# Kernel optimization log

Hardware: AMD Instinct MI355X
Metric: run time of the kernel (lower is better)

The kernel has to match this reference:

```python
import jax, jax.numpy as jnp
import numpy as np

N_S = 4096      # number of sentences
N_K = 8192      # number of knowledge entries
HID = 1024      # settings.hidden_dim
SENT = 1024     # settings.sent_dim


def setup_inputs() -> dict:
    key = jax.random.key(0)
    ks = jax.random.split(key, 6)
    sentences = jax.random.normal(ks[0], (N_S, SENT), dtype=jnp.float32)
    knowledge = jax.random.normal(ks[1], (N_K, 3 * HID), dtype=jnp.float32)
    # Linear params stored as [in, out] for x @ W + b
    Ws = jax.random.normal(ks[2], (SENT, HID), dtype=jnp.float32) * 0.02
    bs = jnp.zeros((HID,), dtype=jnp.float32)
    Wk = jax.random.normal(ks[3], (3 * HID, HID), dtype=jnp.float32) * 0.02
    bk = jnp.zeros((HID,), dtype=jnp.float32)
    return {"sentences": sentences, "knowledge": knowledge,
            "Ws": Ws, "bs": bs, "Wk": Wk, "bk": bk}


def reference(sentences, knowledge, Ws, bs, Wk, bk):
    S = sentences @ Ws + bs                  # [N_s, h]
    K = knowledge @ Wk + bk                  # [N_k, h]
    align_scores = S @ K.T                   # [N_s, N_k]
    # NOTE: softmax over dim=0 (sentence axis), exactly as the torch module
    attentions = jax.nn.softmax(align_scores, axis=0)
    fused = attentions @ knowledge           # [N_s, 3h]
    return (fused, attentions)
```

## Files before the change

kernel.cpp:

```cpp
#include <hip/hip_runtime.h>
#include <hip/hip_bf16.h>
#include <cstdint>
#include <cstddef>

#define N_S 4096
#define N_Kn 8192
#define HID 1024
#define SENT 1024
#define K3 3072

typedef __attribute__((ext_vector_type(4))) float f4;
typedef __attribute__((ext_vector_type(8))) short bf8;
typedef __attribute__((ext_vector_type(4))) short bf4;
typedef unsigned short u16;

__device__ __forceinline__ u16 f2bf(float x) {
    __hip_bfloat16 h = __float2bfloat16(x);
    return __builtin_bit_cast(u16, h);
}
__device__ __forceinline__ float bf2f(u16 u) {
    union { unsigned int u; float f; } v; v.u = ((unsigned int)u) << 16;
    return v.f;
}

__device__ __forceinline__ void gl16(const u16* g, u16* l) {
    __builtin_amdgcn_global_load_lds(
        (const __attribute__((address_space(1))) void*)g,
        (__attribute__((address_space(3))) void*)l, 16, 0, 0);
}

__device__ __forceinline__ int xcd_swz(int bid, int nwg) {
    const int cpx = nwg >> 3;
    return (bid & 7) * cpx + (bid >> 3);
}


__global__ __launch_bounds__(256) void transpose_split_f32(
    const float* __restrict__ in, u16* __restrict__ hi, u16* __restrict__ lo,
    int R, int C)
{
    __shared__ float tile[32][33];
    const int bx = blockIdx.x * 32, by = blockIdx.y * 32;
    const int tx = threadIdx.x & 31, ty = threadIdx.x >> 5;
#pragma unroll
    for (int i = 0; i < 32; i += 8)
        tile[ty + i][tx] = in[(size_t)(by + ty + i) * C + bx + tx];
    __syncthreads();
#pragma unroll
    for (int i = 0; i < 32; i += 8) {
        const float v = tile[tx][ty + i];
        const u16 h = f2bf(v);
        const size_t o = (size_t)(bx + ty + i) * R + by + tx;
        hi[o] = h;
        lo[o] = f2bf(v - bf2f(h));
    }
}

__global__ __launch_bounds__(256) void transpose_f32_bf16(
    const float* __restrict__ in, u16* __restrict__ out, int R, int C)
{
    __shared__ float tile[32][33];
    const int bx = blockIdx.x * 32, by = blockIdx.y * 32;
    const int tx = threadIdx.x & 31, ty = threadIdx.x >> 5;
#pragma unroll
    for (int i = 0; i < 32; i += 8)
        tile[ty + i][tx] = in[(size_t)(by + ty + i) * C + bx + tx];
    __syncthreads();
#pragma unroll
    for (int i = 0; i < 32; i += 8)
        out[(size_t)(bx + ty + i) * R + by + tx] = f2bf(tile[tx][ty + i]);
}

__global__ __launch_bounds__(256) void gemm_pipe(
    const u16* __restrict__ A, const u16* __restrict__ B,
    float* __restrict__ C, int N, int Kd, int gx)
{
    __shared__ u16 sA[2][4096];
    __shared__ u16 sB[2][4096];

    const int swz = xcd_swz(blockIdx.x, gridDim.x);
    const int bx = swz % gx, by = swz / gx;

    const int t = threadIdx.x;
    const int w = t >> 6, l = t & 63;
    const long brow = (long)by * 128, bcol = (long)bx * 128;
    const int grow = l >> 2;
    const int gcol = ((l & 3) ^ ((l >> 3) & 3)) * 8;

    const int wr = (w >> 1) * 64, wc = (w & 1) * 64;
    const int fr = l & 15, kg = l >> 4;
    const int kq = (kg ^ ((fr >> 1) & 3)) * 8;

    const u16* gA0 = A + (brow + w * 16 + grow) * (long)Kd + gcol;
    const u16* gA1 = A + (brow + 64 + w * 16 + grow) * (long)Kd + gcol;
    const u16* gB0 = B + (bcol + w * 16 + grow) * (long)Kd + gcol;
    const u16* gB1 = B + (bcol + 64 + w * 16 + grow) * (long)Kd + gcol;
    const int lb0 = w * 512, lb1 = 2048 + w * 512;

    f4 acc[4][4];
#pragma unroll
    for (int m = 0; m < 4; m++)
#pragma unroll
        for (int n = 0; n < 4; n++) acc[m][n] = (f4){0.f, 0.f, 0.f, 0.f};

    const int nkt = Kd >> 5;

    gl16(gA0, &sA[0][lb0]); gl16(gA1, &sA[0][lb1]);
    gl16(gB0, &sB[0][lb0]); gl16(gB1, &sB[0][lb1]);
    asm volatile("s_waitcnt vmcnt(0)" ::: "memory");
    __builtin_amdgcn_s_barrier();
    asm volatile("" ::: "memory");

    int cur = 0;
    for (int kt = 0; kt < nkt; ++kt) {
        if (kt + 1 < nkt) {
            const long ko = (long)(kt + 1) * 32;
            const int nx = cur ^ 1;
            gl16(gA0 + ko, &sA[nx][lb0]); gl16(gA1 + ko, &sA[nx][lb1]);
            gl16(gB0 + ko, &sB[nx][lb0]); gl16(gB1 + ko, &sB[nx][lb1]);
        }

        bf8 fa[4], fb[4];
#pragma unroll
        for (int m = 0; m < 4; ++m) {
            fa[m] = *(bf8*)&sA[cur][(wr + m * 16 + fr) * 32 + kq];
            fb[m] = *(bf8*)&sB[cur][(wc + m * 16 + fr) * 32 + kq];
        }
#pragma unroll
        for (int m = 0; m < 4; ++m)
#pragma unroll
            for (int n = 0; n < 4; ++n)
                acc[m][n] = __builtin_amdgcn_mfma_f32_16x16x32_bf16(fa[m], fb[n], acc[m][n], 0, 0, 0);

        asm volatile("s_waitcnt vmcnt(0)" ::: "memory");
        __builtin_amdgcn_s_barrier();
        asm volatile("" ::: "memory");
        cur ^= 1;
    }

#pragma unroll
    for (int n = 0; n < 4; ++n) {
        const long c = bcol + wc + n * 16 + fr;
#pragma unroll
        for (int m = 0; m < 4; ++m) {
            const long r0 = brow + wr + m * 16 + kg * 4;
#pragma unroll
            for (int r = 0; r < 4; ++r)
                C[(r0 + r) * (long)N + c] = acc[m][n][r];
        }
    }
}

template <bool SPLIT, bool AF32, bool EPIS>
__global__ __launch_bounds__(256) void gemm_mfma(
    const void* __restrict__ Aany, const u16* __restrict__ Alo_,
    const u16* __restrict__ Bhi_, const u16* __restrict__ Blo_,
    float* __restrict__ Cf, u16* __restrict__ Chi, u16* __restrict__ Clo,
    const float* __restrict__ bias, int N, int Kd, int gx)
{
    constexpr int SA = AF32 ? 48 : 32;
    __shared__ u16 sAh[128 * SA];
    __shared__ u16 sAl[SPLIT ? 128 * SA : 8];
    __shared__ u16 sBh[128 * 32];
    __shared__ u16 sBl[SPLIT ? 128 * 32 : 8];

    const int swz = xcd_swz(blockIdx.x, gridDim.x);
    const int bxi = swz % gx, byi = swz / gx;

    const int t = threadIdx.x;
    const int w = t >> 6;
    const int l = t & 63;
    const long brow = (long)byi * 128;
    const long bcol = (long)bxi * 128;

    const int grow = l >> 2;
    const int gcol = ((l & 3) ^ ((l >> 3) & 3)) * 8;

    const int wr = (w >> 1) * 64;
    const int wc = (w & 1) * 64;
    const int fr = l & 15;
    const int kg = l >> 4;
    const int kq = (kg ^ ((fr >> 1) & 3)) * 8;

    f4 acc[4][4];
#pragma unroll
    for (int m = 0; m < 4; m++)
#pragma unroll
        for (int n = 0; n < 4; n++) acc[m][n] = (f4){0.f, 0.f, 0.f, 0.f};

    const int nkt = Kd >> 5;
    for (int kt = 0; kt < nkt; ++kt) {
        const int k0 = kt * 32;

#pragma unroll
        for (int i = 0; i < 2; ++i) {
            const long r = bcol + i * 64 + w * 16 + grow;
            const int lb = i * 2048 + w * 512;
            gl16(Bhi_ + r * Kd + k0 + gcol, sBh + lb);
            if constexpr (SPLIT) gl16(Blo_ + r * Kd + k0 + gcol, sBl + lb);
        }

        if constexpr (!AF32) {
            const u16* Ahi = (const u16*)Aany;
#pragma unroll
            for (int i = 0; i < 2; ++i) {
                const long r = brow + i * 64 + w * 16 + grow;
                const int lb = i * 2048 + w * 512;
                gl16(Ahi + r * Kd + k0 + gcol, sAh + lb);
                if constexpr (SPLIT) gl16(Alo_ + r * Kd + k0 + gcol, sAl + lb);
            }
        } else {
            const float* Af = (const float*)Aany;
            const int ar = w * 8 + (l >> 3);
            const int cF = (l & 7) * 4;
#pragma unroll
            for (int j = 0; j < 4; ++j) {
                const int r = j * 32 + ar;
                const f4 v = *(const f4*)(Af + (brow + r) * (long)Kd + k0 + cF);
                u16 h[4], lw[4];
#pragma unroll
                for (int q = 0; q < 4; ++q) {
                    h[q] = f2bf(v[q]);
                    if constexpr (SPLIT) lw[q] = f2bf(v[q] - bf2f(h[q]));
                }
                *(bf4*)&sAh[r * SA + cF] = *(bf4*)h;
                if constexpr (SPLIT) *(bf4*)&sAl[r * SA + cF] = *(bf4*)lw;
            }
        }
        __syncthreads();

        bf8 fah[4], fbh[4], fal[4], fbl[4];
#pragma unroll
        for (int m = 0; m < 4; ++m) {
            if constexpr (AF32) {
                fah[m] = *(bf8*)&sAh[(wr + m * 16 + fr) * SA + kg * 8];
                if constexpr (SPLIT) fal[m] = *(bf8*)&sAl[(wr + m * 16 + fr) * SA + kg * 8];
            } else {
                fah[m] = *(bf8*)&sAh[(wr + m * 16 + fr) * 32 + kq];
                if constexpr (SPLIT) fal[m] = *(bf8*)&sAl[(wr + m * 16 + fr) * 32 + kq];
            }
            fbh[m] = *(bf8*)&sBh[(wc + m * 16 + fr) * 32 + kq];
            if constexpr (SPLIT) fbl[m] = *(bf8*)&sBl[(wc + m * 16 + fr) * 32 + kq];
        }
#pragma unroll
        for (int m = 0; m < 4; ++m)
#pragma unroll
            for (int n = 0; n < 4; ++n) {
                acc[m][n] = __builtin_amdgcn_mfma_f32_16x16x32_bf16(fah[m], fbh[n], acc[m][n], 0, 0, 0);
                if constexpr (SPLIT) {
                    acc[m][n] = __builtin_amdgcn_mfma_f32_16x16x32_bf16(fah[m], fbl[n], acc[m][n], 0, 0, 0);
                    acc[m][n] = __builtin_amdgcn_mfma_f32_16x16x32_bf16(fal[m], fbh[n], acc[m][n], 0, 0, 0);
                }
            }
        __syncthreads();
    }

#pragma unroll
    for (int n = 0; n < 4; ++n) {
        const long c = bcol + wc + n * 16 + fr;
        float bv = 0.f;
        if constexpr (EPIS) bv = bias[c];
#pragma unroll
        for (int m = 0; m < 4; ++m) {
            const long r0 = brow + wr + m * 16 + kg * 4;
#pragma unroll
            for (int r = 0; r < 4; ++r) {
                const float v = acc[m][n][r] + bv;
                if constexpr (EPIS) {
                    const u16 h = f2bf(v);
                    Chi[(r0 + r) * (long)N + c] = h;
                    Clo[(r0 + r) * (long)N + c] = f2bf(v - bf2f(h));
                } else {
                    Cf[(r0 + r) * (long)N + c] = v;
                }
            }
        }
    }
}

#define RCHUNK 128

__global__ __launch_bounds__(256) void softmax_partial(
    const float* __restrict__ align, float* __restrict__ pm, float* __restrict__ ps)
{
    const int col = blockIdx.x * 256 + threadIdx.x;
    const int r0 = blockIdx.y * RCHUNK;
    float m = -3.4e38f;
    for (int r = 0; r < RCHUNK; r++)
        m = fmaxf(m, align[(size_t)(r0 + r) * N_Kn + col]);
    float s = 0.f;
    for (int r = 0; r < RCHUNK; r++)
        s += __expf(align[(size_t)(r0 + r) * N_Kn + col] - m);
    pm[(size_t)blockIdx.y * N_Kn + col] = m;
    ps[(size_t)blockIdx.y * N_Kn + col] = s;
}

__global__ __launch_bounds__(256) void softmax_combine(
    const float* __restrict__ pm, const float* __restrict__ ps,
    float* __restrict__ fm, float* __restrict__ fsinv)
{
    const int col = blockIdx.x * 256 + threadIdx.x;
    float m = -3.4e38f;
#pragma unroll
    for (int i = 0; i < 32; i++) m = fmaxf(m, pm[(size_t)i * N_Kn + col]);
    float s = 0.f;
#pragma unroll
    for (int i = 0; i < 32; i++)
        s += ps[(size_t)i * N_Kn + col] * __expf(pm[(size_t)i * N_Kn + col] - m);
    fm[col] = m;
    fsinv[col] = 1.f / s;
}

__global__ __launch_bounds__(256) void softmax_norm(
    float* __restrict__ align, u16* __restrict__ abf,
    const float* __restrict__ fm, const float* __restrict__ fsinv)
{
    const int col = blockIdx.x * 256 + threadIdx.x;
    const int r0 = blockIdx.y * RCHUNK;
    const float m = fm[col], si = fsinv[col];
    for (int r = 0; r < RCHUNK; r++) {
        const size_t idx = (size_t)(r0 + r) * N_Kn + col;
        const float v = __expf(align[idx] - m) * si;
        align[idx] = v;
        abf[idx] = f2bf(v);
    }
}

extern "C" void kernel_launch(void* const* d_in, const int* in_sizes, int n_in,
                              void* d_out, int out_size, void* d_ws, size_t ws_size,
                              hipStream_t stream)
{
    const float* sentences = (const float*)d_in[0];
    const float* knowledge = (const float*)d_in[1];
    const float* Ws = (const float*)d_in[2];
    const float* bs = (const float*)d_in[3];
    const float* Wk = (const float*)d_in[4];
    const float* bk = (const float*)d_in[5];

    float* out_fused = (float*)d_out;
    float* out_attn = (float*)d_out + (size_t)N_S * K3;

    char* w = (char*)d_ws;
    u16* attn_bf = (u16*)w;
    u16* WsT_hi = (u16*)w; w += (size_t)HID * SENT * 2;
    u16* WsT_lo = (u16*)w; w += (size_t)HID * SENT * 2;
    u16* WkT_hi = (u16*)w; w += (size_t)HID * K3 * 2;
    u16* WkT_lo = (u16*)w; w += (size_t)HID * K3 * 2;
    u16* S_hi   = (u16*)w; w += (size_t)N_S * HID * 2;
    u16* S_lo   = (u16*)w; w += (size_t)N_S * HID * 2;
    u16* K_hi   = (u16*)w; w += (size_t)N_Kn * HID * 2;
    u16* K_lo   = (u16*)w; w += (size_t)N_Kn * HID * 2;
    u16* kT     = (u16*)w; w += (size_t)K3 * N_Kn * 2;
    float* pm   = (float*)w; w += (size_t)32 * N_Kn * 4;
    float* ps   = (float*)w; w += (size_t)32 * N_Kn * 4;
    float* fm   = (float*)w; w += (size_t)N_Kn * 4;
    float* fsv  = (float*)w; w += (size_t)N_Kn * 4;

    transpose_split_f32<<<dim3(HID / 32, SENT / 32), 256, 0, stream>>>(Ws, WsT_hi, WsT_lo, SENT, HID);
    transpose_split_f32<<<dim3(HID / 32, K3 / 32), 256, 0, stream>>>(Wk, WkT_hi, WkT_lo, K3, HID);
    transpose_f32_bf16<<<dim3(K3 / 32, N_Kn / 32), 256, 0, stream>>>(knowledge, kT, N_Kn, K3);

    gemm_mfma<true, true, true><<<(HID / 128) * (N_S / 128), 256, 0, stream>>>(
        sentences, nullptr, WsT_hi, WsT_lo, nullptr, S_hi, S_lo, bs, HID, SENT, HID / 128);

    gemm_mfma<true, true, true><<<(HID / 128) * (N_Kn / 128), 256, 0, stream>>>(
        knowledge, nullptr, WkT_hi, WkT_lo, nullptr, K_hi, K_lo, bk, HID, K3, HID / 128);

    gemm_mfma<true, false, false><<<(N_Kn / 128) * (N_S / 128), 256, 0, stream>>>(
        S_hi, S_lo, K_hi, K_lo, out_attn, nullptr, nullptr, nullptr, N_Kn, HID, N_Kn / 128);

    softmax_partial<<<dim3(N_Kn / 256, N_S / RCHUNK), 256, 0, stream>>>(out_attn, pm, ps);
    softmax_combine<<<dim3(N_Kn / 256), 256, 0, stream>>>(pm, ps, fm, fsv);
    softmax_norm<<<dim3(N_Kn / 256, N_S / RCHUNK), 256, 0, stream>>>(out_attn, attn_bf, fm, fsv);

    gemm_pipe<<<(K3 / 128) * (N_S / 128), 256, 0, stream>>>(
        attn_bf, kT, out_fused, K3, N_Kn, K3 / 128);
}
```

Measured before the change: 812.3 us.

## Replace final GEMM with 256x256 eight-wave pipelined kernel and tile-group swizzle

The attention-times-knowledge GEMM moves from 128x128 tiles with 4 waves to 256x256 tiles with 8 waves and a 64-wide K step. Loads are staged in phases interleaved with MFMA work, with s_setprio raised around the MFMA blocks. This raises arithmetic intensity and overlaps global-to-LDS copies with compute. The other MFMA GEMMs now map blocks in 4x4 supertiles for better L2 reuse. The costs are a much larger LDS footprint (128 KB per block) and a grid of only 192 blocks, which may underfill the GPU.

```diff
diff --git a/kernel.cpp b/kernel.cpp
--- a/kernel.cpp
+++ b/kernel.cpp
@@ -33,7 +33,6 @@
     const int cpx = nwg >> 3;
     return (bid & 7) * cpx + (bid >> 3);
 }
-
 
 __global__ __launch_bounds__(256) void transpose_split_f32(
     const float* __restrict__ in, u16* __restrict__ hi, u16* __restrict__ lo,
@@ -71,79 +70,104 @@
         out[(size_t)(bx + ty + i) * R + by + tx] = f2bf(tile[tx][ty + i]);
 }
 
-__global__ __launch_bounds__(256) void gemm_pipe(
+__global__ __launch_bounds__(512, 2) void gemm8(
     const u16* __restrict__ A, const u16* __restrict__ B,
     float* __restrict__ C, int N, int Kd, int gx)
 {
-    __shared__ u16 sA[2][4096];
-    __shared__ u16 sB[2][4096];
+    __shared__ u16 sA[2][2][8192];
+    __shared__ u16 sB[2][2][8192];
 
     const int swz = xcd_swz(blockIdx.x, gridDim.x);
     const int bx = swz % gx, by = swz / gx;
+    const long brow = (long)by * 256, bcol = (long)bx * 256;
 
     const int t = threadIdx.x;
     const int w = t >> 6, l = t & 63;
-    const long brow = (long)by * 128, bcol = (long)bx * 128;
-    const int grow = l >> 2;
-    const int gcol = ((l & 3) ^ ((l >> 3) & 3)) * 8;
-
-    const int wr = (w >> 1) * 64, wc = (w & 1) * 64;
     const int fr = l & 15, kg = l >> 4;
-    const int kq = (kg ^ ((fr >> 1) & 3)) * 8;
-
-    const u16* gA0 = A + (brow + w * 16 + grow) * (long)Kd + gcol;
-    const u16* gA1 = A + (brow + 64 + w * 16 + grow) * (long)Kd + gcol;
-    const u16* gB0 = B + (bcol + w * 16 + grow) * (long)Kd + gcol;
-    const u16* gB1 = B + (bcol + 64 + w * 16 + grow) * (long)Kd + gcol;
-    const int lb0 = w * 512, lb1 = 2048 + w * 512;
-
-    f4 acc[4][4];
-#pragma unroll
-    for (int m = 0; m < 4; m++)
-#pragma unroll
-        for (int n = 0; n < 4; n++) acc[m][n] = (f4){0.f, 0.f, 0.f, 0.f};
-
-    const int nkt = Kd >> 5;
-
-    gl16(gA0, &sA[0][lb0]); gl16(gA1, &sA[0][lb1]);
-    gl16(gB0, &sB[0][lb0]); gl16(gB1, &sB[0][lb1]);
+    const int wm = w >> 2;
+    const int wn = w & 3;
+    const int hb = wn >> 1;
+    const int cb = (wn & 1) * 64;
+
+    const int srow = t >> 3;
+    const int schk = ((t & 7) ^ (srow & 7)) << 3;
+    const int sldb = w << 9;
+
+    auto stage = [&](const u16* g, u16* lds) {
+        gl16(g + (long)srow * Kd + schk, lds + sldb);
+        gl16(g + (long)(srow + 64) * Kd + schk, lds + 4096 + sldb);
+    };
+
+    f4 acc[8][4];
+#pragma unroll
+    for (int m = 0; m < 8; ++m)
+#pragma unroll
+        for (int n = 0; n < 4; ++n) acc[m][n] = (f4){0.f, 0.f, 0.f, 0.f};
+
+    auto phase = [&](int buf, int mh, int nh, int stg, long kts, bool wait) {
+        bf8 fa[4][2], fb[2][2];
+#pragma unroll
+        for (int m = 0; m < 4; ++m)
+#pragma unroll
+            for (int kk = 0; kk < 2; ++kk)
+                fa[m][kk] = *(bf8*)&sA[buf][wm][
+                    (mh * 64 + m * 16 + fr) * 64 + (((kk << 2) + kg) ^ (fr & 7)) * 8];
+#pragma unroll
+        for (int nn = 0; nn < 2; ++nn)
+#pragma unroll
+            for (int kk = 0; kk < 2; ++kk)
+                fb[nn][kk] = *(bf8*)&sB[buf][hb][
+                    (cb + nh * 32 + nn * 16 + fr) * 64 + (((kk << 2) + kg) ^ (fr & 7)) * 8];
+        if (stg == 1) {
+            stage(A + brow * Kd + kts, &sA[buf ^ 1][0][0]);
+            stage(A + (brow + 128) * Kd + kts, &sA[buf ^ 1][1][0]);
+        } else if (stg == 2) {
+            stage(B + bcol * Kd + kts, &sB[buf ^ 1][0][0]);
+            stage(B + (bcol + 128) * Kd + kts, &sB[buf ^ 1][1][0]);
+        }
+        __builtin_amdgcn_s_barrier();
+        __builtin_amdgcn_s_setprio(1);
+#pragma unroll
+        for (int kk = 0; kk < 2; ++kk)
+#pragma unroll
+            for (int m = 0; m < 4; ++m)
+#pragma unroll
+                for (int nn = 0; nn < 2; ++nn)
+                    acc[mh * 4 + m][nh * 2 + nn] = __builtin_amdgcn_mfma_f32_16x16x32_bf16(
+                        fa[m][kk], fb[nn][kk], acc[mh * 4 + m][nh * 2 + nn], 0, 0, 0);
+        __builtin_amdgcn_s_setprio(0);
+        if (wait) asm volatile("s_waitcnt vmcnt(0)" ::: "memory");
+        __builtin_amdgcn_s_barrier();
+    };
+
+    stage(A + brow * Kd, &sA[0][0][0]);
+    stage(A + (brow + 128) * Kd, &sA[0][1][0]);
+    stage(B + bcol * Kd, &sB[0][0][0]);
+    stage(B + (bcol + 128) * Kd, &sB[0][1][0]);
     asm volatile("s_waitcnt vmcnt(0)" ::: "memory");
     __builtin_amdgcn_s_barrier();
-    asm volatile("" ::: "memory");
-
-    int cur = 0;
-    for (int kt = 0; kt < nkt; ++kt) {
-        if (kt + 1 < nkt) {
-            const long ko = (long)(kt + 1) * 32;
-            const int nx = cur ^ 1;
-            gl16(gA0 + ko, &sA[nx][lb0]); gl16(gA1 + ko, &sA[nx][lb1]);
-            gl16(gB0 + ko, &sB[nx][lb0]); gl16(gB1 + ko, &sB[nx][lb1]);
-        }
-
-        bf8 fa[4], fb[4];
-#pragma unroll
-        for (int m = 0; m < 4; ++m) {
-            fa[m] = *(bf8*)&sA[cur][(wr + m * 16 + fr) * 32 + kq];
-            fb[m] = *(bf8*)&sB[cur][(wc + m * 16 + fr) * 32 + kq];
-        }
-#pragma unroll
-        for (int m = 0; m < 4; ++m)
-#pragma unroll
-            for (int n = 0; n < 4; ++n)
-                acc[m][n] = __builtin_amdgcn_mfma_f32_16x16x32_bf16(fa[m], fb[n], acc[m][n], 0, 0, 0);
-
-        asm volatile("s_waitcnt vmcnt(0)" ::: "memory");
-        __builtin_amdgcn_s_barrier();
-        asm volatile("" ::: "memory");
-        cur ^= 1;
+
+    const int NIT = Kd >> 7;
+    for (int it = 0; it < NIT; ++it) {
+        const long k1 = ((long)(2 * it + 1)) << 6;
+        const long k2 = ((long)(2 * it + 2)) << 6;
+        const bool more = (it + 1 < NIT);
+        phase(0, 0, 0, 1, k1, false);
+        phase(0, 0, 1, 2, k1, false);
+        phase(0, 1, 0, 0, 0, false);
+        phase(0, 1, 1, 0, 0, true);
+        phase(1, 0, 0, more ? 1 : 0, k2, false);
+        phase(1, 0, 1, more ? 2 : 0, k2, false);
+        phase(1, 1, 0, 0, 0, false);
+        phase(1, 1, 1, 0, 0, true);
     }
 
 #pragma unroll
     for (int n = 0; n < 4; ++n) {
-        const long c = bcol + wc + n * 16 + fr;
-#pragma unroll
-        for (int m = 0; m < 4; ++m) {
-            const long r0 = brow + wr + m * 16 + kg * 4;
+        const long c = bcol + wn * 64 + n * 16 + fr;
+#pragma unroll
+        for (int m = 0; m < 8; ++m) {
+            const long r0 = brow + wm * 128 + m * 16 + kg * 4;
 #pragma unroll
             for (int r = 0; r < 4; ++r)
                 C[(r0 + r) * (long)N + c] = acc[m][n][r];
@@ -165,7 +189,10 @@
     __shared__ u16 sBl[SPLIT ? 128 * 32 : 8];
 
     const int swz = xcd_swz(blockIdx.x, gridDim.x);
-    const int bxi = swz % gx, byi = swz / gx;
+    const int nst_x = gx >> 2;
+    const int st = swz >> 4, off = swz & 15;
+    const int bxi = (st % nst_x) * 4 + (off & 3);
+    const int byi = (st / nst_x) * 4 + (off >> 2);
 
     const int t = threadIdx.x;
     const int w = t >> 6;
@@ -373,6 +400,6 @@
     softmax_combine<<<dim3(N_Kn / 256), 256, 0, stream>>>(pm, ps, fm, fsv);
     softmax_norm<<<dim3(N_Kn / 256, N_S / RCHUNK), 256, 0, stream>>>(out_attn, attn_bf, fm, fsv);
 
-    gemm_pipe<<<(K3 / 128) * (N_S / 128), 256, 0, stream>>>(
-        attn_bf, kT, out_fused, K3, N_Kn, K3 / 128);
-}
+    gemm8<<<(K3 / 256) * (N_S / 256), 512, 0, stream>>>(
+        attn_bf, kT, out_fused, K3, N_Kn, K3 / 256);
+}
```

After: 829.9 us. +2.2%, slower.
